# Optimization experiments

Hardware: AMD Instinct MI355X
Metric: run time of the kernel (lower is better)

Reference implementation:

```python
import jax, jax.numpy as jnp
import numpy as np
from jax import lax

HID = 128
NGRAPH = 64  # ligands per receptor


def _conv3d(x, w, b):
    # x: [N,C,D,H,W], w: [O,I,3,3,3], VALID padding (torch Conv3d default)
    y = lax.conv_general_dilated(x, w, (1, 1, 1), 'VALID',
                                 dimension_numbers=('NCDHW', 'OIDHW', 'NCDHW'))
    return y + b[None, :, None, None, None]


def setup_inputs() -> dict:
    key = jax.random.key(0)
    ks = jax.random.split(key, 40)
    i = iter(range(40))
    rn = lambda shape, s=1.0: jax.random.normal(ks[next(i)], shape, jnp.float32) * s
    W = 0.02
    inp = {
        'ms_feat_0': rn((4, 32, 16, 16, 16)),
        'ms_feat_1': rn((4, 64, 8, 8, 8)),
        'token_features': rn((4, 128, 256)),
        'lig_atom': rn((4, 1024, 64)),
        'lig_graph': rn((4, NGRAPH, 64)),
        'ligand_batch': jnp.sort(jax.random.randint(ks[next(i)], (1024,), 0, NGRAPH)).astype(jnp.int32),
        # token_mlp
        'W_token': rn((256, HID), W), 'b_token': jnp.zeros((HID,)),
        # pocket_mlp_list (reversed order: conv0 <- ms_feat_1 C=64, conv1 <- ms_feat_0 C=32)
        'Wc0': rn((HID, 64, 3, 3, 3), W), 'bc0': jnp.zeros((HID,)),
        'Wc1': rn((HID, 32, 3, 3, 3), W), 'bc1': jnp.zeros((HID,)),
        # pocket_mlp
        'W_pocket': rn((2 * HID, HID), W), 'b_pocket': jnp.zeros((HID,)),
        # concat layer / gate
        'W_cat': rn((3 * HID, HID), W), 'b_cat': jnp.zeros((HID,)),
        'W_gate': rn((3 * HID, HID), W), 'b_gate': jnp.zeros((HID,)),
        # ligand projections
        'W_atom': rn((64, HID), W), 'b_atom': jnp.zeros((HID,)),
        'W_graph': rn((64, HID), W), 'b_graph': jnp.zeros((HID,)),
        # energy bias mlp
        'W_bias1': rn((2 * HID, HID), W), 'b_bias1': jnp.zeros((HID,)),
        'W_bias2': rn((HID, 1), W), 'b_bias2': jnp.zeros((1,)),
        # interaction mlp + pair energy / gate
        'W_int': rn((HID, HID), W), 'b_int': jnp.zeros((HID,)),
        'W_pe': rn((HID, 1), W), 'b_pe': jnp.zeros((1,)),
        'W_pg': rn((HID, 1), W), 'b_pg': jnp.zeros((1,)),
    }
    return inp


def reference(ms_feat_0, ms_feat_1, token_features, lig_atom, lig_graph, ligand_batch,
              W_token, b_token, Wc0, bc0, Wc1, bc1, W_pocket, b_pocket,
              W_cat, b_cat, W_gate, b_gate, W_atom, b_atom, W_graph, b_graph,
              W_bias1, b_bias1, W_bias2, b_bias2, W_int, b_int,
              W_pe, b_pe, W_pg, b_pg):
    silu = jax.nn.silu
    lrelu = lambda x: jax.nn.leaky_relu(x, 0.01)

    # ---- ready_to_calculate ----
    # reversed multi-scale: [ms_feat_1, ms_feat_0]; SiLU -> Conv3d -> spatial mean
    p0 = _conv3d(silu(ms_feat_1), Wc0, bc0).mean(axis=(2, 3, 4))  # [N,HID]
    p1 = _conv3d(silu(ms_feat_0), Wc1, bc1).mean(axis=(2, 3, 4))  # [N,HID]
    pocket = silu(jnp.concatenate([p0, p1], -1)) @ W_pocket + b_pocket  # [N,HID]

    tok = silu(token_features) @ W_token + b_token                # [N,Nt,HID]
    tok_agg = jnp.concatenate([tok.sum(1), tok.mean(1)], -1)      # [N,2*HID]

    pf = jnp.concatenate([pocket, tok_agg], -1)                   # [N,3*HID]
    pf = (pf @ W_cat + b_cat) * jax.nn.sigmoid(pf @ W_gate + b_gate)  # [N,HID]

    # ---- per-image affinity (vectorized over images) ----
    atoms = lig_atom @ W_atom + b_atom                            # [N,Na,HID]
    # einsum('ik,jk->ijk') outer interaction map, batched over images
    imap = jnp.einsum('nik,njk->nijk', atoms, tok)                # [N,Na,Nt,HID]
    h = lrelu(imap @ W_int + b_int)                               # [N,Na,Nt,HID]
    pe = (h @ W_pe + b_pe) * jax.nn.sigmoid(h @ W_pg + b_pg)      # [N,Na,Nt,1]
    atom_e = pe.sum(axis=(2, 3))                                  # [N,Na]
    seg = jax.vmap(lambda v: jax.ops.segment_sum(v, ligand_batch, num_segments=NGRAPH))(atom_e)  # [N,Ng]

    gf = lig_graph @ W_graph + b_graph                            # [N,Ng,HID]
    pf_rep = jnp.broadcast_to(pf[:, None, :], gf.shape)           # [N,Ng,HID]
    z = jnp.concatenate([pf_rep, gf], -1)                         # [N,Ng,2*HID]
    bias = lrelu(z @ W_bias1 + b_bias1) @ W_bias2 + b_bias2       # [N,Ng,1]

    return seg + bias[..., 0]                                     # [N,Ng]
```

## Files before the change

kernel.cpp:

```cpp
#include <hip/hip_runtime.h>
#include <hip/hip_bf16.h>

#define NIMG 4

typedef __attribute__((ext_vector_type(8))) short short8v;
typedef __attribute__((ext_vector_type(4))) float float4v;
typedef __attribute__((ext_vector_type(4))) int   int4v;

__device__ __forceinline__ float sigm(float x){ return 1.f/(1.f+__expf(-x)); }
__device__ __forceinline__ float silu(float x){ return x/(1.f+__expf(-x)); }
__device__ __forceinline__ float lrelu(float x){ return fmaxf(x, 0.01f*x); }
__device__ __forceinline__ unsigned short f2bf(float f){
  union { float f; unsigned int i; } v; v.f = f;
  unsigned int r = v.i + 0x7fffu + ((v.i>>16)&1u);
  return (unsigned short)(r>>16); }

template<int CTRL>
__device__ __forceinline__ float dpp_radd(float v){
  int s = __builtin_amdgcn_update_dpp(0, __builtin_bit_cast(int, v), CTRL, 0xF, 0xF, true);
  return v + __builtin_bit_cast(float, s);
}
__device__ __forceinline__ float row16_reduce(float v){
  v = dpp_radd<0x128>(v);
  v = dpp_radd<0x124>(v);
  v = dpp_radd<0x122>(v);
  v = dpp_radd<0x121>(v);
  return v;
}

__device__ __forceinline__ short8v scale_frag(short8v a, const float* tv){
  int4v ai = __builtin_bit_cast(int4v, a);
  int4v oi;
  #pragma unroll
  for(int p=0;p<4;p++){
    float lo = __builtin_bit_cast(float, ai[p] << 16);
    float hi = __builtin_bit_cast(float, (int)(ai[p] & 0xFFFF0000));
    lo *= tv[2*p]; hi *= tv[2*p+1];
    int r;
    asm("v_cvt_pk_bf16_f32 %0, %1, %2" : "=v"(r) : "v"(lo), "v"(hi));
    oi[p] = r;
  }
  return __builtin_bit_cast(short8v, oi);
}

template<int DIM, int ODIM>
__device__ void wsum_body(const float* __restrict__ x, float* __restrict__ S,
                          int vb, float* sh){
  const float* xp = x + (size_t)vb*(DIM*DIM*DIM);
  for(int p=threadIdx.x; p<DIM*DIM*DIM; p+=256) sh[p] = silu(xp[p]);
  __syncthreads();
  const int wave = threadIdx.x>>6, lane = threadIdx.x&63;
  for(int tap=wave; tap<27; tap+=4){
    const int kd=tap/9, kh=(tap/3)%3, kw=tap%3;
    const int base = kd*DIM*DIM + kh*DIM + kw;
    float ps = 0.f;
    for(int idx=lane; idx<ODIM*ODIM*ODIM; idx+=64){
      int od = idx/(ODIM*ODIM); int r = idx - od*(ODIM*ODIM);
      int oh = r/ODIM; int ow = r - oh*ODIM;
      ps += sh[base + od*DIM*DIM + oh*DIM + ow];
    }
    #pragma unroll
    for(int m=32;m>=1;m>>=1) ps += __shfl_xor(ps,m);
    if(lane==0) S[vb*27 + tap] = ps;
  }
}

__global__ __launch_bounds__(256) void k_pre(
    const float* __restrict__ tf, const float* __restrict__ Wtok,
    const float* __restrict__ btok, float* __restrict__ tok,
    const float* __restrict__ ms1, float* __restrict__ S1,
    const float* __restrict__ ms0, float* __restrict__ S0,
    const float* __restrict__ la, const float* __restrict__ Wa,
    const float* __restrict__ ba, unsigned short* __restrict__ atoms_bf,
    float* __restrict__ atom_e,
    const float* __restrict__ Wint, unsigned short* __restrict__ Wt){
  __shared__ float sh[4096];
  const int b = blockIdx.x;
  const int tid = threadIdx.x;
  if(b < 512){
    const int row = b;
    sh[tid] = silu(tf[row*256 + tid]);
    __syncthreads();
    const int c = tid & 127, sg = tid >> 7;
    float acc = 0.f;
    #pragma unroll 8
    for(int q=sg*128; q<sg*128+128; q++) acc = fmaf(sh[q], Wtok[q*128+c], acc);
    if(sg==1) sh[256+c] = acc;
    __syncthreads();
    if(sg==0) tok[row*128+c] = acc + sh[256+c] + btok[c];
  } else if(b < 768){
    wsum_body<8,6>(ms1, S1, b-512, sh);
  } else if(b < 896){
    wsum_body<16,14>(ms0, S0, b-768, sh);
  } else if(b < 2944){
    const int rowb = (b-896)*2;
    if(tid < 128) sh[tid] = la[(size_t)rowb*64 + tid];
    __syncthreads();
    const int r2 = tid>>7, c = tid&127;
    const float* s = sh + r2*64;
    float acc = ba[c];
    #pragma unroll 8
    for(int k=0;k<64;k++) acc = fmaf(s[k], Wa[k*128+c], acc);
    atoms_bf[(size_t)(rowb+r2)*128 + c] = f2bf(acc);
    if(tid<2) atom_e[rowb+tid] = 0.f;
  } else {
    const int idx = (b-2944)*256 + tid;
    const int c = idx >> 7, k = idx & 127;
    Wt[c*128 + k] = f2bf(Wint[k*128 + c]);
  }
}

__global__ void k_pconv(const float* __restrict__ S1, const float* __restrict__ S0,
                        const float* __restrict__ Wc0, const float* __restrict__ bc0,
                        const float* __restrict__ Wc1, const float* __restrict__ bc1,
                        const float* __restrict__ tok, float* __restrict__ toksum,
                        float* __restrict__ pp){
  const int b = blockIdx.x;
  const int n = b >> 7, c = b & 127;
  const int tid = threadIdx.x;
  float a0 = 0.f, a1 = 0.f, ts = 0.f;
  { const float* w = Wc0 + c*1728; const float* s = S1 + n*1728;
    for(int q=tid; q<1728; q+=256) a0 = fmaf(w[q], s[q], a0); }
  { const float* w = Wc1 + c*864;  const float* s = S0 + n*864;
    for(int q=tid; q<864; q+=256)  a1 = fmaf(w[q], s[q], a1); }
  for(int j=tid; j<128; j+=256) ts = tok[(n*128+j)*128 + c];
  #pragma unroll
  for(int m=32;m>=1;m>>=1){
    a0 += __shfl_xor(a0,m); a1 += __shfl_xor(a1,m); ts += __shfl_xor(ts,m);
  }
  __shared__ float r0[4], r1[4], r2[4];
  if((tid&63)==0){ r0[tid>>6]=a0; r1[tid>>6]=a1; r2[tid>>6]=ts; }
  __syncthreads();
  if(tid==0){
    float p0 = bc0[c] + (r0[0]+r0[1]+r0[2]+r0[3])*(1.f/216.f);
    float p1 = bc1[c] + (r1[0]+r1[1]+r1[2]+r1[3])*(1.f/2744.f);
    pp[n*256 + c]       = silu(p0);
    pp[n*256 + 128 + c] = silu(p1);
    toksum[n*128 + c]   = r2[0]+r2[1]+r2[2]+r2[3];
  }
}

__global__ void k_pf2(const float* __restrict__ pp, const float* __restrict__ toksum,
                      const float* __restrict__ Wp,  const float* __restrict__ bp,
                      const float* __restrict__ Wcat, const float* __restrict__ bcat,
                      const float* __restrict__ Wgate,const float* __restrict__ bgate,
                      float* __restrict__ pf){
  __shared__ float ps[256];
  __shared__ float zz[384];
  __shared__ float part[4][128];
  __shared__ float partg[4][128];
  const int n = blockIdx.x;
  const int tid = threadIdx.x;
  const int c = tid & 127, s = tid >> 7;
  if(tid < 256) ps[tid] = pp[n*256 + tid];
  __syncthreads();
  float a = 0.f;
  for(int q=s*64; q<s*64+64; q++) a = fmaf(ps[q], Wp[q*128+c], a);
  part[s][c] = a;
  __syncthreads();
  if(s==0){
    float pk = bp[c] + part[0][c]+part[1][c]+part[2][c]+part[3][c];
    float ts = toksum[n*128+c];
    zz[c] = pk; zz[128+c] = ts; zz[256+c] = ts*(1.f/128.f);
  }
  __syncthreads();
  float a1=0.f, a2=0.f;
  for(int q=s*96; q<s*96+96; q++){
    float z = zz[q];
    a1 = fmaf(z, Wcat[q*128+c], a1);
    a2 = fmaf(z, Wgate[q*128+c], a2);
  }
  part[s][c]=a1; partg[s][c]=a2;
  __syncthreads();
  if(s==0){
    float v1 = bcat[c] +part[0][c]+part[1][c]+part[2][c]+part[3][c];
    float v2 = bgate[c]+partg[0][c]+partg[1][c]+partg[2][c]+partg[3][c];
    pf[n*128+c] = v1 * sigm(v2);
  }
}

__global__ __launch_bounds__(256,2) void k_inter(
    const unsigned short* __restrict__ atoms_bf,
    const float* __restrict__ tok,
    const unsigned short* __restrict__ Wt,
    const float* __restrict__ bint,
    const float* __restrict__ Wpe, const float* __restrict__ bpe,
    const float* __restrict__ Wpg, const float* __restrict__ bpg,
    float* __restrict__ atom_e){
  __shared__ float red[2*2*2*32*2];

  const int b0 = blockIdx.x;
  const int bid = (b0 & 7)*128 + (b0 >> 3);
  const int n = bid >> 8;
  const int chunk = (bid >> 4) & 15;
  const int jg = bid & 15;
  const int tid = threadIdx.x;
  const int w = tid >> 6, lane = tid & 63;
  const int t = lane & 15, q = lane >> 4;
  const int g = w >> 1, wc = w & 1;

  const int rbase = n*1024 + chunk*64;

  short8v areg[2][4];
  { const unsigned short* ab = atoms_bf + (size_t)(rbase + g*32 + t)*128 + q*8;
    #pragma unroll
    for(int fr=0;fr<2;fr++)
      #pragma unroll
      for(int ks=0;ks<4;ks++)
        areg[fr][ks] = *(const short8v*)(ab + fr*16*128 + ks*32);
  }
  short8v breg[4][4];
  { const unsigned short* wb = Wt + (size_t)(wc*64 + t)*128 + q*8;
    #pragma unroll
    for(int fc=0;fc<4;fc++)
      #pragma unroll
      for(int ks=0;ks<4;ks++)
        breg[fc][ks] = *(const short8v*)(wb + fc*16*128 + ks*32);
  }
  float bi[4], wpe[4], wpg[4];
  #pragma unroll
  for(int fc=0;fc<4;fc++){
    int cc = wc*64 + fc*16 + t;
    bi[fc]=bint[cc]; wpe[fc]=Wpe[cc]; wpg[fc]=Wpg[cc];
  }
  const float bpe0 = bpe[0], bpg0 = bpg[0];
  const float* tokn = tok + (size_t)(n*128 + jg*8)*128 + q*8;

  float peacc = 0.f;

  for(int j=0;j<8;j++){
    const int jb = j & 1;
    float trv[4][8];
    { const float* tr = tokn + j*128;
      #pragma unroll
      for(int ks=0;ks<4;ks++){
        *(float4v*)&trv[ks][0] = *(const float4v*)(tr + ks*32);
        *(float4v*)&trv[ks][4] = *(const float4v*)(tr + ks*32 + 4);
      }
    }
    float4v acc[2][4];
    #pragma unroll
    for(int fr=0;fr<2;fr++)
      #pragma unroll
      for(int fc=0;fc<4;fc++)
        acc[fr][fc] = (float4v){bi[fc],bi[fc],bi[fc],bi[fc]};
    #pragma unroll
    for(int ks=0;ks<4;ks++){
      short8v s0 = scale_frag(areg[0][ks], trv[ks]);
      short8v s1 = scale_frag(areg[1][ks], trv[ks]);
      #pragma unroll
      for(int fc=0;fc<4;fc++){
        acc[0][fc] = __builtin_amdgcn_mfma_f32_16x16x32_bf16(s0, breg[fc][ks], acc[0][fc], 0,0,0);
        acc[1][fc] = __builtin_amdgcn_mfma_f32_16x16x32_bf16(s1, breg[fc][ks], acc[1][fc], 0,0,0);
      }
    }
    #pragma unroll
    for(int fr=0;fr<2;fr++){
      #pragma unroll
      for(int r=0;r<4;r++){
        float d1=0.f, d2=0.f;
        #pragma unroll
        for(int fc=0;fc<4;fc++){
          float h = lrelu(acc[fr][fc][r]);
          d1 = fmaf(h, wpe[fc], d1);
          d2 = fmaf(h, wpg[fc], d2);
        }
        d1 = row16_reduce(d1);
        d2 = row16_reduce(d2);
        if(t==0){
          int a = fr*16 + q*4 + r;
          float* rp = red + (((jb*2+g)*2+wc)*32 + a)*2;
          rp[0] = d1; rp[1] = d2;
        }
      }
    }
    __syncthreads();
    if(wc==0 && lane<32){
      const float* rp = red + (((jb*2+g)*2+0)*32 + lane)*2;
      const float* rq = red + (((jb*2+g)*2+1)*32 + lane)*2;
      float d1 = rp[0]+rq[0], d2 = rp[1]+rq[1];
      peacc += (d1 + bpe0) * sigm(d2 + bpg0);
    }
  }
  if(wc==0 && lane<32) atomicAdd(atom_e + rbase + g*32 + lane, peacc);
}

__global__ void k_bias_seg(const float* __restrict__ lg, const float* __restrict__ Wg,
                       const float* __restrict__ bg, const float* __restrict__ pf,
                       const float* __restrict__ W1, const float* __restrict__ b1,
                       const float* __restrict__ W2, const float* __restrict__ b2,
                       const float* __restrict__ atom_e, const int* __restrict__ batch,
                       float* __restrict__ out){
  __shared__ float row[64];
  __shared__ float z[256];
  __shared__ float red[128];
  __shared__ float red2[128];
  const int b = blockIdx.x;
  const int n = b >> 6, g = b & 63;
  const int c = threadIdx.x;
  if(c < 64) row[c] = lg[b*64 + c];
  __syncthreads();
  float gf = bg[c];
  #pragma unroll 8
  for(int k=0;k<64;k++) gf = fmaf(row[k], Wg[k*128+c], gf);
  z[c] = pf[n*128+c]; z[128+c] = gf;
  __syncthreads();
  float tacc = b1[c];
  for(int qq=0;qq<256;qq++) tacc = fmaf(z[qq], W1[qq*128+c], tacc);
  tacc = lrelu(tacc);
  float s = 0.f;
  const float* ae = atom_e + n*1024;
  for(int i=c;i<1024;i+=128){ float v = ae[i]; s += (batch[i]==g) ? v : 0.f; }
  red[c] = tacc * W2[c];
  red2[c] = s;
  __syncthreads();
  for(int st=64; st>0; st>>=1){
    if(c<st){ red[c]+=red[c+st]; red2[c]+=red2[c+st]; }
    __syncthreads();
  }
  if(c==0) out[b] = red[0] + b2[0] + red2[0];
}

extern "C" void kernel_launch(void* const* d_in, const int* in_sizes, int n_in,
                              void* d_out, int out_size, void* d_ws, size_t ws_size,
                              hipStream_t stream) {
  const float* ms0   = (const float*)d_in[0];
  const float* ms1   = (const float*)d_in[1];
  const float* tfeat = (const float*)d_in[2];
  const float* la    = (const float*)d_in[3];
  const float* lg    = (const float*)d_in[4];
  const int*   batch = (const int*)  d_in[5];
  const float* Wtok  = (const float*)d_in[6];
  const float* btok  = (const float*)d_in[7];
  const float* Wc0   = (const float*)d_in[8];
  const float* bc0   = (const float*)d_in[9];
  const float* Wc1   = (const float*)d_in[10];
  const float* bc1   = (const float*)d_in[11];
  const float* Wp    = (const float*)d_in[12];
  const float* bp    = (const float*)d_in[13];
  const float* Wcat  = (const float*)d_in[14];
  const float* bcat  = (const float*)d_in[15];
  const float* Wgate = (const float*)d_in[16];
  const float* bgate = (const float*)d_in[17];
  const float* Wa    = (const float*)d_in[18];
  const float* ba    = (const float*)d_in[19];
  const float* Wgr   = (const float*)d_in[20];
  const float* bgr   = (const float*)d_in[21];
  const float* W1    = (const float*)d_in[22];
  const float* b1    = (const float*)d_in[23];
  const float* W2    = (const float*)d_in[24];
  const float* b2    = (const float*)d_in[25];
  const float* Wint  = (const float*)d_in[26];
  const float* bint  = (const float*)d_in[27];
  const float* Wpe   = (const float*)d_in[28];
  const float* bpe   = (const float*)d_in[29];
  const float* Wpg   = (const float*)d_in[30];
  const float* bpg   = (const float*)d_in[31];
  float* out = (float*)d_out;

  float* ws      = (float*)d_ws;
  float* tok     = ws;
  float* S1      = ws + 65536;
  float* S0      = S1 + 6912;
  float* pp      = S0 + 3456;
  float* pf      = pp + 1024;
  float* toksum  = pf + 512;
  float* atom_e  = toksum + 512;
  unsigned short* atoms_bf = (unsigned short*)(atom_e + 4096);
  unsigned short* Wt       = atoms_bf + 524288;

  k_pre<<<3008, 256, 0, stream>>>(tfeat, Wtok, btok, tok,
                                  ms1, S1, ms0, S0,
                                  la, Wa, ba, atoms_bf, atom_e,
                                  Wint, Wt);
  k_inter<<<1024, 256, 0, stream>>>(atoms_bf, tok, Wt, bint,
                                    Wpe, bpe, Wpg, bpg, atom_e);
  k_pconv<<<NIMG*128, 256, 0, stream>>>(S1, S0, Wc0, bc0, Wc1, bc1,
                                        tok, toksum, pp);
  k_pf2<<<NIMG, 512, 0, stream>>>(pp, toksum, Wp, bp, Wcat, bcat, Wgate, bgate, pf);
  k_bias_seg<<<NIMG*64, 128, 0, stream>>>(lg, Wgr, bgr, pf, W1, b1, W2, b2,
                                          atom_e, batch, out);
}
```

Before: 215.5 us.

## Switch interaction MFMA to fp16 with packed scaling and defer per-token reductions

Atoms and the transposed W_int are now stored in fp16, and token values are packed to fp16 so the outer-product scaling is one v_pk_mul_f16 per pair instead of unpack, multiply and repack from bf16. The MFMA becomes the f16 variant. The per-token shared-memory barrier inside the j loop is removed: partials for all 8 tokens go to a larger shared buffer and are combined once after the loop. k_bias_seg is widened to 256 threads with split-K partials and a wave-shuffle reduction. fp16 has narrower range than bf16 and the round-toward-zero pack adds error, which risks accuracy for large activations.

```diff
diff --git a/kernel.cpp b/kernel.cpp
--- a/kernel.cpp
+++ b/kernel.cpp
@@ -3,17 +3,14 @@
 
 #define NIMG 4
 
-typedef __attribute__((ext_vector_type(8))) short short8v;
+typedef __attribute__((ext_vector_type(8))) _Float16 half8v;
+typedef __attribute__((ext_vector_type(2))) _Float16 half2v;
 typedef __attribute__((ext_vector_type(4))) float float4v;
 typedef __attribute__((ext_vector_type(4))) int   int4v;
 
 __device__ __forceinline__ float sigm(float x){ return 1.f/(1.f+__expf(-x)); }
 __device__ __forceinline__ float silu(float x){ return x/(1.f+__expf(-x)); }
 __device__ __forceinline__ float lrelu(float x){ return fmaxf(x, 0.01f*x); }
-__device__ __forceinline__ unsigned short f2bf(float f){
-  union { float f; unsigned int i; } v; v.f = f;
-  unsigned int r = v.i + 0x7fffu + ((v.i>>16)&1u);
-  return (unsigned short)(r>>16); }
 
 template<int CTRL>
 __device__ __forceinline__ float dpp_radd(float v){
@@ -28,19 +25,16 @@
   return v;
 }
 
-__device__ __forceinline__ short8v scale_frag(short8v a, const float* tv){
+__device__ __forceinline__ half8v scale_frag16(half8v a, const int* tpk){
   int4v ai = __builtin_bit_cast(int4v, a);
   int4v oi;
   #pragma unroll
   for(int p=0;p<4;p++){
-    float lo = __builtin_bit_cast(float, ai[p] << 16);
-    float hi = __builtin_bit_cast(float, (int)(ai[p] & 0xFFFF0000));
-    lo *= tv[2*p]; hi *= tv[2*p+1];
     int r;
-    asm("v_cvt_pk_bf16_f32 %0, %1, %2" : "=v"(r) : "v"(lo), "v"(hi));
+    asm("v_pk_mul_f16 %0, %1, %2" : "=v"(r) : "v"(ai[p]), "v"(tpk[p]));
     oi[p] = r;
   }
-  return __builtin_bit_cast(short8v, oi);
+  return __builtin_bit_cast(half8v, oi);
 }
 
 template<int DIM, int ODIM>
@@ -71,7 +65,7 @@
     const float* __restrict__ ms1, float* __restrict__ S1,
     const float* __restrict__ ms0, float* __restrict__ S0,
     const float* __restrict__ la, const float* __restrict__ Wa,
-    const float* __restrict__ ba, unsigned short* __restrict__ atoms_bf,
+    const float* __restrict__ ba, unsigned short* __restrict__ atoms_h,
     float* __restrict__ atom_e,
     const float* __restrict__ Wint, unsigned short* __restrict__ Wt){
   __shared__ float sh[4096];
@@ -101,12 +95,12 @@
     float acc = ba[c];
     #pragma unroll 8
     for(int k=0;k<64;k++) acc = fmaf(s[k], Wa[k*128+c], acc);
-    atoms_bf[(size_t)(rowb+r2)*128 + c] = f2bf(acc);
+    atoms_h[(size_t)(rowb+r2)*128 + c] = __builtin_bit_cast(unsigned short, (_Float16)acc);
     if(tid<2) atom_e[rowb+tid] = 0.f;
   } else {
     const int idx = (b-2944)*256 + tid;
     const int c = idx >> 7, k = idx & 127;
-    Wt[c*128 + k] = f2bf(Wint[k*128 + c]);
+    Wt[c*128 + k] = __builtin_bit_cast(unsigned short, (_Float16)(Wint[k*128 + c]));
   }
 }
 
@@ -180,14 +174,14 @@
 }
 
 __global__ __launch_bounds__(256,2) void k_inter(
-    const unsigned short* __restrict__ atoms_bf,
+    const unsigned short* __restrict__ atoms_h,
     const float* __restrict__ tok,
     const unsigned short* __restrict__ Wt,
     const float* __restrict__ bint,
     const float* __restrict__ Wpe, const float* __restrict__ bpe,
     const float* __restrict__ Wpg, const float* __restrict__ bpg,
     float* __restrict__ atom_e){
-  __shared__ float red[2*2*2*32*2];
+  __shared__ float red[8][2][2][32][2];
 
   const int b0 = blockIdx.x;
   const int bid = (b0 & 7)*128 + (b0 >> 3);
@@ -201,21 +195,21 @@
 
   const int rbase = n*1024 + chunk*64;
 
-  short8v areg[2][4];
-  { const unsigned short* ab = atoms_bf + (size_t)(rbase + g*32 + t)*128 + q*8;
+  half8v areg[2][4];
+  { const unsigned short* ab = atoms_h + (size_t)(rbase + g*32 + t)*128 + q*8;
     #pragma unroll
     for(int fr=0;fr<2;fr++)
       #pragma unroll
       for(int ks=0;ks<4;ks++)
-        areg[fr][ks] = *(const short8v*)(ab + fr*16*128 + ks*32);
-  }
-  short8v breg[4][4];
+        areg[fr][ks] = *(const half8v*)(ab + fr*16*128 + ks*32);
+  }
+  half8v breg[4][4];
   { const unsigned short* wb = Wt + (size_t)(wc*64 + t)*128 + q*8;
     #pragma unroll
     for(int fc=0;fc<4;fc++)
       #pragma unroll
       for(int ks=0;ks<4;ks++)
-        breg[fc][ks] = *(const short8v*)(wb + fc*16*128 + ks*32);
+        breg[fc][ks] = *(const half8v*)(wb + fc*16*128 + ks*32);
   }
   float bi[4], wpe[4], wpg[4];
   #pragma unroll
@@ -226,16 +220,18 @@
   const float bpe0 = bpe[0], bpg0 = bpg[0];
   const float* tokn = tok + (size_t)(n*128 + jg*8)*128 + q*8;
 
-  float peacc = 0.f;
-
+  #pragma unroll
   for(int j=0;j<8;j++){
-    const int jb = j & 1;
-    float trv[4][8];
+    int tpk[4][4];
     { const float* tr = tokn + j*128;
       #pragma unroll
       for(int ks=0;ks<4;ks++){
-        *(float4v*)&trv[ks][0] = *(const float4v*)(tr + ks*32);
-        *(float4v*)&trv[ks][4] = *(const float4v*)(tr + ks*32 + 4);
+        float4v t0 = *(const float4v*)(tr + ks*32);
+        float4v t1 = *(const float4v*)(tr + ks*32 + 4);
+        tpk[ks][0] = __builtin_bit_cast(int, __builtin_amdgcn_cvt_pkrtz(t0[0],t0[1]));
+        tpk[ks][1] = __builtin_bit_cast(int, __builtin_amdgcn_cvt_pkrtz(t0[2],t0[3]));
+        tpk[ks][2] = __builtin_bit_cast(int, __builtin_amdgcn_cvt_pkrtz(t1[0],t1[1]));
+        tpk[ks][3] = __builtin_bit_cast(int, __builtin_amdgcn_cvt_pkrtz(t1[2],t1[3]));
       }
     }
     float4v acc[2][4];
@@ -246,12 +242,12 @@
         acc[fr][fc] = (float4v){bi[fc],bi[fc],bi[fc],bi[fc]};
     #pragma unroll
     for(int ks=0;ks<4;ks++){
-      short8v s0 = scale_frag(areg[0][ks], trv[ks]);
-      short8v s1 = scale_frag(areg[1][ks], trv[ks]);
+      half8v s0 = scale_frag16(areg[0][ks], tpk[ks]);
+      half8v s1 = scale_frag16(areg[1][ks], tpk[ks]);
       #pragma unroll
       for(int fc=0;fc<4;fc++){
-        acc[0][fc] = __builtin_amdgcn_mfma_f32_16x16x32_bf16(s0, breg[fc][ks], acc[0][fc], 0,0,0);
-        acc[1][fc] = __builtin_amdgcn_mfma_f32_16x16x32_bf16(s1, breg[fc][ks], acc[1][fc], 0,0,0);
+        acc[0][fc] = __builtin_amdgcn_mfma_f32_16x16x32_f16(s0, breg[fc][ks], acc[0][fc], 0,0,0);
+        acc[1][fc] = __builtin_amdgcn_mfma_f32_16x16x32_f16(s1, breg[fc][ks], acc[1][fc], 0,0,0);
       }
     }
     #pragma unroll
@@ -269,56 +265,68 @@
         d2 = row16_reduce(d2);
         if(t==0){
           int a = fr*16 + q*4 + r;
-          float* rp = red + (((jb*2+g)*2+wc)*32 + a)*2;
-          rp[0] = d1; rp[1] = d2;
+          red[j][g][wc][a][0] = d1;
+          red[j][g][wc][a][1] = d2;
         }
       }
     }
-    __syncthreads();
-    if(wc==0 && lane<32){
-      const float* rp = red + (((jb*2+g)*2+0)*32 + lane)*2;
-      const float* rq = red + (((jb*2+g)*2+1)*32 + lane)*2;
-      float d1 = rp[0]+rq[0], d2 = rp[1]+rq[1];
-      peacc += (d1 + bpe0) * sigm(d2 + bpg0);
-    }
-  }
-  if(wc==0 && lane<32) atomicAdd(atom_e + rbase + g*32 + lane, peacc);
-}
-
-__global__ void k_bias_seg(const float* __restrict__ lg, const float* __restrict__ Wg,
-                       const float* __restrict__ bg, const float* __restrict__ pf,
-                       const float* __restrict__ W1, const float* __restrict__ b1,
-                       const float* __restrict__ W2, const float* __restrict__ b2,
-                       const float* __restrict__ atom_e, const int* __restrict__ batch,
-                       float* __restrict__ out){
+  }
+  __syncthreads();
+  if(tid < 64){
+    const int gg = tid >> 5, a = tid & 31;
+    float s_ = 0.f;
+    #pragma unroll
+    for(int j=0;j<8;j++){
+      float d1 = red[j][gg][0][a][0] + red[j][gg][1][a][0];
+      float d2 = red[j][gg][0][a][1] + red[j][gg][1][a][1];
+      s_ += (d1 + bpe0) * sigm(d2 + bpg0);
+    }
+    atomicAdd(atom_e + rbase + tid, s_);
+  }
+}
+
+__global__ __launch_bounds__(256) void k_bias_seg(
+    const float* __restrict__ lg, const float* __restrict__ Wg,
+    const float* __restrict__ bg, const float* __restrict__ pf,
+    const float* __restrict__ W1, const float* __restrict__ b1,
+    const float* __restrict__ W2, const float* __restrict__ b2,
+    const float* __restrict__ atom_e, const int* __restrict__ batch,
+    float* __restrict__ out){
   __shared__ float row[64];
   __shared__ float z[256];
-  __shared__ float red[128];
-  __shared__ float red2[128];
+  __shared__ float partA[128];
+  __shared__ float partB[128];
+  __shared__ float wred[4];
   const int b = blockIdx.x;
   const int n = b >> 6, g = b & 63;
-  const int c = threadIdx.x;
-  if(c < 64) row[c] = lg[b*64 + c];
-  __syncthreads();
-  float gf = bg[c];
+  const int tid = threadIdx.x;
+  const int c = tid & 127, s = tid >> 7;
+  if(tid < 64) row[tid] = lg[b*64 + tid];
+  __syncthreads();
+  float gf = 0.f;
   #pragma unroll 8
-  for(int k=0;k<64;k++) gf = fmaf(row[k], Wg[k*128+c], gf);
-  z[c] = pf[n*128+c]; z[128+c] = gf;
-  __syncthreads();
-  float tacc = b1[c];
-  for(int qq=0;qq<256;qq++) tacc = fmaf(z[qq], W1[qq*128+c], tacc);
-  tacc = lrelu(tacc);
-  float s = 0.f;
+  for(int k=s*32;k<s*32+32;k++) gf = fmaf(row[k], Wg[k*128+c], gf);
+  if(s==1) partA[c] = gf;
+  __syncthreads();
+  if(s==0){ z[c] = pf[n*128+c]; z[128+c] = gf + partA[c] + bg[c]; }
+  __syncthreads();
+  float tacc = 0.f;
+  for(int qq=s*128; qq<s*128+128; qq++) tacc = fmaf(z[qq], W1[qq*128+c], tacc);
+  if(s==1) partB[c] = tacc;
+  float se = 0.f;
   const float* ae = atom_e + n*1024;
-  for(int i=c;i<1024;i+=128){ float v = ae[i]; s += (batch[i]==g) ? v : 0.f; }
-  red[c] = tacc * W2[c];
-  red2[c] = s;
-  __syncthreads();
-  for(int st=64; st>0; st>>=1){
-    if(c<st){ red[c]+=red[c+st]; red2[c]+=red2[c+st]; }
-    __syncthreads();
-  }
-  if(c==0) out[b] = red[0] + b2[0] + red2[0];
+  for(int i=tid;i<1024;i+=256){ float v = ae[i]; se += (batch[i]==g) ? v : 0.f; }
+  __syncthreads();
+  float val = se;
+  if(s==0){
+    float tf = lrelu(tacc + partB[c] + b1[c]);
+    val += tf * W2[c];
+  }
+  #pragma unroll
+  for(int m=32;m>=1;m>>=1) val += __shfl_xor(val,m);
+  if((tid&63)==0) wred[tid>>6] = val;
+  __syncthreads();
+  if(tid==0) out[b] = wred[0]+wred[1]+wred[2]+wred[3] + b2[0];
 }
 
 extern "C" void kernel_launch(void* const* d_in, const int* in_sizes, int n_in,
@@ -366,18 +374,18 @@
   float* pf      = pp + 1024;
   float* toksum  = pf + 512;
   float* atom_e  = toksum + 512;
-  unsigned short* atoms_bf = (unsigned short*)(atom_e + 4096);
-  unsigned short* Wt       = atoms_bf + 524288;
+  unsigned short* atoms_h = (unsigned short*)(atom_e + 4096);
+  unsigned short* Wt      = atoms_h + 524288;
 
   k_pre<<<3008, 256, 0, stream>>>(tfeat, Wtok, btok, tok,
                                   ms1, S1, ms0, S0,
-                                  la, Wa, ba, atoms_bf, atom_e,
+                                  la, Wa, ba, atoms_h, atom_e,
                                   Wint, Wt);
-  k_inter<<<1024, 256, 0, stream>>>(atoms_bf, tok, Wt, bint,
+  k_inter<<<1024, 256, 0, stream>>>(atoms_h, tok, Wt, bint,
                                     Wpe, bpe, Wpg, bpg, atom_e);
   k_pconv<<<NIMG*128, 256, 0, stream>>>(S1, S0, Wc0, bc0, Wc1, bc1,
                                         tok, toksum, pp);
   k_pf2<<<NIMG, 512, 0, stream>>>(pp, toksum, Wp, bp, Wcat, bcat, Wgate, bgate, pf);
-  k_bias_seg<<<NIMG*64, 128, 0, stream>>>(lg, Wgr, bgr, pf, W1, b1, W2, b2,
+  k_bias_seg<<<NIMG*64, 256, 0, stream>>>(lg, Wgr, bgr, pf, W1, b1, W2, b2,
                                           atom_e, batch, out);
 }
```

Result: slower. 235.3 us (+9.2%).
